# Kernel optimization log

Measured on AMD Instinct MI355X. Metric: run time of the kernel, lower is better.

Reference implementation:

```python
import jax, jax.numpy as jnp
import numpy as np

SEQ_LEN, BATCH, INPUT_SIZE, HIDDEN_SIZE = 512, 64, 1024, 1024


def setup_inputs() -> dict:
    key = jax.random.key(0)
    k1, k2, k3 = jax.random.split(key, 3)
    inp = jax.random.normal(k1, (SEQ_LEN, BATCH, INPUT_SIZE), dtype=jnp.float32)
    weight_ih = jax.random.normal(k2, (4 * HIDDEN_SIZE, INPUT_SIZE), dtype=jnp.float32) * 0.01
    weight_hh = jax.random.normal(k3, (4 * HIDDEN_SIZE, HIDDEN_SIZE), dtype=jnp.float32) * 0.01
    bias_ih = jnp.zeros((4 * HIDDEN_SIZE,), dtype=jnp.float32)
    bias_hh = jnp.zeros((4 * HIDDEN_SIZE,), dtype=jnp.float32)
    h0 = jnp.zeros((BATCH, HIDDEN_SIZE), dtype=jnp.float32)
    c0 = jnp.zeros((BATCH, HIDDEN_SIZE), dtype=jnp.float32)
    return {"input": inp, "weight_ih": weight_ih, "weight_hh": weight_hh,
            "bias_ih": bias_ih, "bias_hh": bias_hh, "h0": h0, "c0": c0}


def _lstm(input, weight_ih, weight_hh, bias_ih, bias_hh, h0, c0):
    H = weight_hh.shape[1]
    # Precompute input projections for all timesteps in one big GEMM: [T,B,4H]
    x_proj = jnp.einsum('tbi,gi->tbg', input, weight_ih) + bias_ih + bias_hh

    def step(carry, xg_t):
        h_prev, c_prev = carry
        gates = xg_t + h_prev @ weight_hh.T  # [B, 4H]
        i_g = jax.nn.sigmoid(gates[:, 0*H:1*H])
        f_g = jax.nn.sigmoid(gates[:, 1*H:2*H])
        g_g = jnp.tanh(gates[:, 2*H:3*H])
        o_g = jax.nn.sigmoid(gates[:, 3*H:4*H])
        c_cur = f_g * c_prev + i_g * g_g
        h_cur = o_g * jnp.tanh(c_cur)
        return (h_cur, c_cur), h_cur

    (h_last, c_last), outputs = jax.lax.scan(step, (h0, c0), x_proj)
    return outputs, (h_last[None], c_last[None])


def reference(input, weight_ih, weight_hh, bias_ih, bias_hh, h0, c0):
    return _lstm(input, weight_ih, weight_hh, bias_ih, bias_hh, h0, c0)
```

## Files before the change

kernel.cpp:

```cpp
#include <hip/hip_runtime.h>
#include <stdint.h>

#define SEQ    512
#define NBATCH 64
#define HID    1024
#define GDIM   4096

typedef __attribute__((ext_vector_type(4))) float          f32x4;
typedef __attribute__((ext_vector_type(8))) short          s16x8;
typedef __attribute__((ext_vector_type(4))) unsigned short u16x4;
typedef __attribute__((ext_vector_type(4))) unsigned int   u32x4;

#define MFMA_BF16(a,b,c) __builtin_amdgcn_mfma_f32_16x16x32_bf16((a),(b),(c),0,0,0)

__device__ __forceinline__ unsigned short f2bf(float f){
  union { float f; unsigned u; } v; v.f = f;
  unsigned r = v.u + 0x7fffu + ((v.u >> 16) & 1u);
  return (unsigned short)(r >> 16);
}

__device__ __forceinline__ void gload_lds16(const void* g, void* l){
  __builtin_amdgcn_global_load_lds((const __attribute__((address_space(1))) void*)g,
                                   (__attribute__((address_space(3))) void*)l,
                                   16, 0, 0);
}

__global__ __launch_bounds__(256) void cvt_bf16(const float* __restrict__ s,
                                                unsigned short* __restrict__ d, int n4){
  int i = blockIdx.x*256 + threadIdx.x;
  if (i >= n4) return;
  f32x4 v = *(const f32x4*)(s + (size_t)i*4);
  u16x4 o;
  o[0]=f2bf(v[0]); o[1]=f2bf(v[1]); o[2]=f2bf(v[2]); o[3]=f2bf(v[3]);
  *(u16x4*)(d + (size_t)i*4) = o;
}

__global__ __launch_bounds__(256) void init_state(const float* __restrict__ h0,
                                                  const float* __restrict__ c0,
                                                  unsigned short* __restrict__ hring,
                                                  float* __restrict__ cstate){
  int i = blockIdx.x*256 + threadIdx.x;
  hring[i]  = f2bf(h0[i]);
  cstate[i] = c0[i];
}

__global__ __launch_bounds__(256,1) void gemm_xproj(
    const unsigned short* __restrict__ A,
    const unsigned short* __restrict__ Bw,
    const float* __restrict__ bih, const float* __restrict__ bhh,
    float* __restrict__ C, int M)
{
  __shared__ unsigned short Al[2][128*64];
  __shared__ unsigned short Bl[2][128*64];

  const int bm = blockIdx.x >> 5;
  const int bn = blockIdx.x & 31;
  const int tid = threadIdx.x;
  const int wv = tid >> 6, l = tid & 63;
  const int wm = wv >> 1, wn = wv & 1;
  const int c16 = l & 15, rq = l >> 4;

  const unsigned short* Ab = A  + (size_t)bm*128*1024;
  const unsigned short* Bb = Bw + (size_t)bn*128*1024;

  f32x4 acc[4][4];
#pragma unroll
  for (int i=0;i<4;++i)
#pragma unroll
    for (int j=0;j<4;++j) acc[i][j] = (f32x4){0.f,0.f,0.f,0.f};

  auto stage = [&](int buf, int kt){
    const int k0 = kt*64;
    const int rsub = wv*8 + (l>>3);
    const int col  = (l&7)*8;
#pragma unroll
    for (int is=0; is<4; ++is){
      const int row = is*32 + rsub;
      gload_lds16(Ab + (size_t)row*1024 + k0 + col, &Al[buf][row*64 + col]);
      gload_lds16(Bb + (size_t)row*1024 + k0 + col, &Bl[buf][row*64 + col]);
    }
  };

  stage(0, 0);
  asm volatile("s_waitcnt vmcnt(0)" ::: "memory");
  __syncthreads();

  for (int kt = 0; kt < 16; ++kt){
    const int cur = kt & 1;
    if (kt < 15) stage(cur^1, kt+1);
#pragma unroll
    for (int ks=0; ks<2; ++ks){
      s16x8 afr[4], bfr[4];
#pragma unroll
      for (int mi=0;mi<4;++mi)
        afr[mi] = *(const s16x8*)&Al[cur][(wm*64 + mi*16 + c16)*64 + ks*32 + rq*8];
#pragma unroll
      for (int ni=0;ni<4;++ni)
        bfr[ni] = *(const s16x8*)&Bl[cur][(wn*64 + ni*16 + c16)*64 + ks*32 + rq*8];
#pragma unroll
      for (int mi=0;mi<4;++mi)
#pragma unroll
        for (int ni=0;ni<4;++ni)
          acc[mi][ni] = MFMA_BF16(afr[mi], bfr[ni], acc[mi][ni]);
    }
    asm volatile("s_waitcnt vmcnt(0)" ::: "memory");
    __syncthreads();
  }

  const int crow0 = bm*128 + wm*64;
  const int ccol0 = bn*128 + wn*64;
#pragma unroll
  for (int ni=0;ni<4;++ni){
    const int col = ccol0 + ni*16 + c16;
    const float bsum = bih[col] + bhh[col];
#pragma unroll
    for (int mi=0;mi<4;++mi){
      const int row = crow0 + mi*16 + rq*4;
#pragma unroll
      for (int r=0;r<4;++r)
        C[(size_t)(row+r)*GDIM + col] = acc[mi][ni][r] + bsum;
    }
  }
}

__global__ __launch_bounds__(512,1) void lstm_rec(
    const unsigned short* __restrict__ whhb,
    const float* __restrict__ xproj,
    unsigned short* __restrict__ hring,
    float* __restrict__ cstate,
    float* __restrict__ outp,
    unsigned int* __restrict__ bar,
    int t0, int nsteps)
{
  const int tid = threadIdx.x;
  const int wv = tid >> 6, l = tid & 63;
  const int kq = wv >> 1, rh = wv & 1;
  const int c16 = l & 15, rq = l >> 4;
  const int bq = blockIdx.x >> 6;
  const int hg = blockIdx.x & 63;
  const int hc0 = hg * 16;
  const int b0  = bq * 16;
  const int eb = tid >> 4, ec = tid & 15;
  const int sb = tid >> 5, cl0 = tid & 31;

  __shared__ s16x8 hls[16*128];
  __shared__ float part[8*16*36];
  __shared__ __align__(16) unsigned short hsh[16*16];

  s16x8 breg[2][8];
#pragma unroll
  for (int nt = 0; nt < 2; ++nt)
#pragma unroll
    for (int ks = 0; ks < 8; ++ks){
      const int n = rh*32 + nt*16 + c16;
      const int grow = (n & 3)*HID + hc0 + (n >> 2);
      const int k = kq*256 + ks*32 + rq*8;
      breg[nt][ks] = *(const s16x8*)(whhb + (size_t)grow*HID + k);
    }

  float creg = 0.f, xp[4] = {0.f,0.f,0.f,0.f};
  if (tid < 256){
    creg = cstate[(size_t)(b0+eb)*HID + hc0 + ec];
#pragma unroll
    for (int g = 0; g < 4; ++g)
      xp[g] = xproj[(size_t)(b0+eb)*GDIM + g*HID + hc0 + ec];
  }

  const unsigned int* myflag = bar + ((bq*64 + l) << 5);

  for (int t = t0; t < t0 + nsteps; ++t){
    if (wv == 0){
      unsigned fv; int spins = 0;
      const unsigned ut = (unsigned)t;
      do {
        asm volatile("global_load_dword %0, %1, off sc0 sc1\n\ts_waitcnt vmcnt(0)"
                     : "=v"(fv) : "v"(myflag) : "memory");
        if (fv >= ut) break;
        if (++spins > 4) __builtin_amdgcn_s_sleep(1);
      } while (spins < (1 << 17));
    }
    __syncthreads();

    {
      const unsigned short* gb = hring + (size_t)(t & 1)*65536
                               + (size_t)(b0 + sb)*HID;
      u32x4 tmp[4];
#pragma unroll
      for (int i = 0; i < 4; ++i){
        const unsigned short* p = gb + (cl0 + 32*i)*8;
        asm volatile("global_load_dwordx4 %0, %1, off sc0 sc1"
                     : "=v"(tmp[i]) : "v"(p));
      }
      asm volatile("s_waitcnt vmcnt(0)" ::: "memory");
      __builtin_amdgcn_sched_barrier(0);
#pragma unroll
      for (int i = 0; i < 4; ++i){
        const int cl = cl0 + 32*i;
        hls[sb*128 + ((cl & ~7) | ((cl & 7) ^ (sb & 7)))] =
            __builtin_bit_cast(s16x8, tmp[i]);
      }
    }
    __syncthreads();

    f32x4 acc0 = (f32x4){0.f,0.f,0.f,0.f};
    f32x4 acc1 = (f32x4){0.f,0.f,0.f,0.f};
    {
      s16x8 af[8];
#pragma unroll
      for (int ks = 0; ks < 8; ++ks){
        const int c = kq*32 + ks*4 + rq;
        af[ks] = hls[c16*128 + ((c & ~7) | ((c & 7) ^ (c16 & 7)))];
      }
#pragma unroll
      for (int ks = 0; ks < 8; ++ks){
        acc0 = MFMA_BF16(af[ks], breg[0][ks], acc0);
        acc1 = MFMA_BF16(af[ks], breg[1][ks], acc1);
      }
    }
#pragma unroll
    for (int r = 0; r < 4; ++r){
      part[wv*576 + (rq*4+r)*36 +      c16] = acc0[r];
      part[wv*576 + (rq*4+r)*36 + 16 + c16] = acc1[r];
    }
    __syncthreads();

    float hval = 0.f;
    if (tid < 256){
      float v[4];
#pragma unroll
      for (int g = 0; g < 4; ++g){
        const int row = ec*4 + g;
        const int pl = (row >> 5);
        const int nl = row & 31;
        v[g] = xp[g]
             + part[(0*2 + pl)*576 + eb*36 + nl]
             + part[(1*2 + pl)*576 + eb*36 + nl]
             + part[(2*2 + pl)*576 + eb*36 + nl]
             + part[(3*2 + pl)*576 + eb*36 + nl];
      }
      const float ig = 1.f/(1.f + __expf(-v[0]));
      const float fg = 1.f/(1.f + __expf(-v[1]));
      const float gg = tanhf(v[2]);
      const float og = 1.f/(1.f + __expf(-v[3]));
      creg = fg*creg + ig*gg;
      hval = og * tanhf(creg);
      hsh[eb*16 + ec] = f2bf(hval);
    }
    __syncthreads();

    if (tid < 32){
      const int row = tid >> 1, half = tid & 1;
      const unsigned short* hp = hring + (size_t)((t+1) & 1)*65536
                               + (size_t)(b0 + row)*HID + hc0 + half*8;
      u32x4 hv = *(const u32x4*)&hsh[row*16 + half*8];
      asm volatile("global_store_dwordx4 %0, %1, off sc0 sc1"
                   :: "v"(hp), "v"(hv) : "memory");
      asm volatile("s_waitcnt vmcnt(0)" ::: "memory");
      if (tid == 0){
        unsigned int* fp = bar + ((bq*64 + hg) << 5);
        unsigned int fv = (unsigned int)(t + 1);
        asm volatile("global_store_dword %0, %1, off sc0 sc1"
                     :: "v"(fp), "v"(fv) : "memory");
      }
    }

    if (tid < 256){
      const size_t oidx = (size_t)(b0+eb)*HID + hc0 + ec;
      outp[(size_t)t*65536 + oidx] = hval;
      if (t == SEQ-1){
        outp[(size_t)SEQ*65536 + oidx]         = hval;
        outp[(size_t)SEQ*65536 + 65536 + oidx] = creg;
      }
      if (t+1 < t0 + nsteps){
        const size_t xrow = (size_t)(t+1 - t0)*NBATCH + (b0+eb);
#pragma unroll
        for (int g = 0; g < 4; ++g)
          xp[g] = xproj[xrow*GDIM + g*HID + hc0 + ec];
      }
    }
  }

  if (tid < 256)
    cstate[(size_t)(b0+eb)*HID + hc0 + ec] = creg;
}

extern "C" void kernel_launch(void* const* d_in, const int* in_sizes, int n_in,
                              void* d_out, int out_size, void* d_ws, size_t ws_size,
                              hipStream_t stream)
{
  const float* inp = (const float*)d_in[0];
  const float* wih = (const float*)d_in[1];
  const float* whh = (const float*)d_in[2];
  const float* bih = (const float*)d_in[3];
  const float* bhh = (const float*)d_in[4];
  const float* h0  = (const float*)d_in[5];
  const float* c0  = (const float*)d_in[6];
  float* outp = (float*)d_out;

  auto alignup = [](size_t x){ return (x + 255) & ~(size_t)255; };
  auto need = [&](size_t ch)->size_t{
    size_t s = 0;
    s += alignup(ch*64*4096*4);
    s += alignup(ch*64*1024*2);
    s += alignup((size_t)4096*1024*2);
    s += alignup((size_t)4096*1024*2);
    s += alignup((size_t)2*64*1024*2);
    s += alignup((size_t)64*1024*4);
    s += alignup((size_t)256*32*4);
    return s;
  };
  int CH = 512;
  while (CH > 2 && need(CH) > ws_size) CH >>= 1;

  char* w = (char*)d_ws;
  float*          xproj  = (float*)w;          w += alignup((size_t)CH*64*4096*4);
  unsigned short* in_bf  = (unsigned short*)w; w += alignup((size_t)CH*64*1024*2);
  unsigned short* wih_bf = (unsigned short*)w; w += alignup((size_t)4096*1024*2);
  unsigned short* whh_bf = (unsigned short*)w; w += alignup((size_t)4096*1024*2);
  unsigned short* hring  = (unsigned short*)w; w += alignup((size_t)2*64*1024*2);
  float*          cst    = (float*)w;          w += alignup((size_t)64*1024*4);
  unsigned int*   bar    = (unsigned int*)w;

  hipMemsetAsync(bar, 0, 256*32*4, stream);

  cvt_bf16<<<4096, 256, 0, stream>>>(wih, wih_bf, 4096*1024/4);
  cvt_bf16<<<4096, 256, 0, stream>>>(whh, whh_bf, 4096*1024/4);
  init_state<<<256, 256, 0, stream>>>(h0, c0, hring, cst);

  const int nch = SEQ / CH;
  for (int ci = 0; ci < nch; ++ci){
    const int t0 = ci * CH;
    const int n4 = CH*64*1024/4;
    cvt_bf16<<<(n4+255)/256, 256, 0, stream>>>(inp + (size_t)t0*65536, in_bf, n4);
    gemm_xproj<<<dim3((CH*64/128)*32), 256, 0, stream>>>(in_bf, wih_bf, bih, bhh,
                                                         xproj, CH*64);
    lstm_rec<<<dim3(256), dim3(512), 0, stream>>>(whh_bf, xproj, hring, cst, outp,
                                                  bar, t0, CH);
  }
}
```

Baseline: 2.203 ms.

## Retile recurrent LSTM blocks to 8 batch rows by 32 hidden units

Each block of the persistent recurrent kernel now handles 8 batch rows and 32 hidden units instead of 16 and 16. Each wave now keeps twice as many W_hh fragments in registers and runs four MFMA tiles per k-step, with the unused half of the 16-row A tile zero-padded in LDS. Each block now polls only 32 producer flags and reads half as much of the h ring per step, which cuts the cross-block synchronisation and global h traffic per step. In exchange, register pressure doubles and half of every MFMA is spent on the padding rows.

```diff
diff --git a/kernel.cpp b/kernel.cpp
--- a/kernel.cpp
+++ b/kernel.cpp
@@ -136,40 +136,42 @@
   const int wv = tid >> 6, l = tid & 63;
   const int kq = wv >> 1, rh = wv & 1;
   const int c16 = l & 15, rq = l >> 4;
-  const int bq = blockIdx.x >> 6;
-  const int hg = blockIdx.x & 63;
-  const int hc0 = hg * 16;
-  const int b0  = bq * 16;
-  const int eb = tid >> 4, ec = tid & 15;
-  const int sb = tid >> 5, cl0 = tid & 31;
+  const int bq = blockIdx.x >> 5;
+  const int hg = blockIdx.x & 31;
+  const int hc0 = hg * 32;
+  const int b0  = bq * 8;
+  const int em = tid >> 5, ec = tid & 31;
+  const int sb = tid >> 6, scl = tid & 63;
 
   __shared__ s16x8 hls[16*128];
-  __shared__ float part[8*16*36];
-  __shared__ __align__(16) unsigned short hsh[16*16];
-
-  s16x8 breg[2][8];
-#pragma unroll
-  for (int nt = 0; nt < 2; ++nt)
-#pragma unroll
-    for (int ks = 0; ks < 8; ++ks){
-      const int n = rh*32 + nt*16 + c16;
-      const int grow = (n & 3)*HID + hc0 + (n >> 2);
-      const int k = kq*256 + ks*32 + rq*8;
-      breg[nt][ks] = *(const s16x8*)(whhb + (size_t)grow*HID + k);
-    }
+  __shared__ float part[4*8*4*33];
+  __shared__ __align__(16) unsigned short hsh[8*32];
+
+  s16x8 breg[4][8];
+#pragma unroll
+  for (int nt = 0; nt < 4; ++nt){
+    const int n = rh*64 + nt*16 + c16;
+    const size_t grow = (size_t)(n & 3)*HID + hc0 + (n >> 2);
+#pragma unroll
+    for (int ks = 0; ks < 8; ++ks)
+      breg[nt][ks] = *(const s16x8*)(whhb + grow*HID + kq*256 + ks*32 + rq*8);
+  }
+
+  hls[1024 + tid] = (s16x8){0,0,0,0,0,0,0,0};
+  hls[1536 + tid] = (s16x8){0,0,0,0,0,0,0,0};
 
   float creg = 0.f, xp[4] = {0.f,0.f,0.f,0.f};
   if (tid < 256){
-    creg = cstate[(size_t)(b0+eb)*HID + hc0 + ec];
+    creg = cstate[(size_t)(b0+em)*HID + hc0 + ec];
 #pragma unroll
     for (int g = 0; g < 4; ++g)
-      xp[g] = xproj[(size_t)(b0+eb)*GDIM + g*HID + hc0 + ec];
-  }
-
-  const unsigned int* myflag = bar + ((bq*64 + l) << 5);
+      xp[g] = xproj[(size_t)(b0+em)*GDIM + g*HID + hc0 + ec];
+  }
+
+  const unsigned int* myflag = bar + ((bq*32 + (l & 31)) << 5);
 
   for (int t = t0; t < t0 + nsteps; ++t){
-    if (wv == 0){
+    if (wv == 0 && l < 32){
       unsigned fv; int spins = 0;
       const unsigned ut = (unsigned)t;
       do {
@@ -184,43 +186,42 @@
     {
       const unsigned short* gb = hring + (size_t)(t & 1)*65536
                                + (size_t)(b0 + sb)*HID;
-      u32x4 tmp[4];
-#pragma unroll
-      for (int i = 0; i < 4; ++i){
-        const unsigned short* p = gb + (cl0 + 32*i)*8;
-        asm volatile("global_load_dwordx4 %0, %1, off sc0 sc1"
-                     : "=v"(tmp[i]) : "v"(p));
-      }
+      u32x4 t0v, t1v;
+      asm volatile("global_load_dwordx4 %0, %1, off sc0 sc1"
+                   : "=v"(t0v) : "v"(gb + scl*8));
+      asm volatile("global_load_dwordx4 %0, %1, off sc0 sc1"
+                   : "=v"(t1v) : "v"(gb + (scl + 64)*8));
       asm volatile("s_waitcnt vmcnt(0)" ::: "memory");
       __builtin_amdgcn_sched_barrier(0);
-#pragma unroll
-      for (int i = 0; i < 4; ++i){
-        const int cl = cl0 + 32*i;
-        hls[sb*128 + ((cl & ~7) | ((cl & 7) ^ (sb & 7)))] =
-            __builtin_bit_cast(s16x8, tmp[i]);
-      }
-    }
-    __syncthreads();
-
-    f32x4 acc0 = (f32x4){0.f,0.f,0.f,0.f};
-    f32x4 acc1 = (f32x4){0.f,0.f,0.f,0.f};
-    {
-      s16x8 af[8];
-#pragma unroll
-      for (int ks = 0; ks < 8; ++ks){
-        const int c = kq*32 + ks*4 + rq;
-        af[ks] = hls[c16*128 + ((c & ~7) | ((c & 7) ^ (c16 & 7)))];
-      }
-#pragma unroll
-      for (int ks = 0; ks < 8; ++ks){
-        acc0 = MFMA_BF16(af[ks], breg[0][ks], acc0);
-        acc1 = MFMA_BF16(af[ks], breg[1][ks], acc1);
-      }
-    }
-#pragma unroll
-    for (int r = 0; r < 4; ++r){
-      part[wv*576 + (rq*4+r)*36 +      c16] = acc0[r];
-      part[wv*576 + (rq*4+r)*36 + 16 + c16] = acc1[r];
+      const int c0 = scl, c1 = scl + 64;
+      hls[sb*128 + ((c0 & ~7) | ((c0 & 7) ^ (sb & 7)))] = __builtin_bit_cast(s16x8, t0v);
+      hls[sb*128 + ((c1 & ~7) | ((c1 & 7) ^ (sb & 7)))] = __builtin_bit_cast(s16x8, t1v);
+    }
+    __syncthreads();
+
+    f32x4 acc[4];
+#pragma unroll
+    for (int nt = 0; nt < 4; ++nt) acc[nt] = (f32x4){0.f,0.f,0.f,0.f};
+#pragma unroll
+    for (int ks = 0; ks < 8; ++ks){
+      const int c = kq*32 + ks*4 + rq;
+      const s16x8 af = hls[c16*128 + ((c & ~7) | ((c & 7) ^ (c16 & 7)))];
+#pragma unroll
+      for (int nt = 0; nt < 4; ++nt)
+        acc[nt] = MFMA_BF16(af, breg[nt][ks], acc[nt]);
+    }
+
+    if (rq < 2){
+#pragma unroll
+      for (int nt = 0; nt < 4; ++nt){
+        const int g = c16 & 3;
+        const int cl = rh*16 + nt*4 + (c16 >> 2);
+#pragma unroll
+        for (int r = 0; r < 4; ++r){
+          const int m = rq*4 + r;
+          part[((kq*8 + m)*4 + g)*33 + cl] = acc[nt][r];
+        }
+      }
     }
     __syncthreads();
 
@@ -229,14 +230,11 @@
       float v[4];
 #pragma unroll
       for (int g = 0; g < 4; ++g){
-        const int row = ec*4 + g;
-        const int pl = (row >> 5);
-        const int nl = row & 31;
         v[g] = xp[g]
-             + part[(0*2 + pl)*576 + eb*36 + nl]
-             + part[(1*2 + pl)*576 + eb*36 + nl]
-             + part[(2*2 + pl)*576 + eb*36 + nl]
-             + part[(3*2 + pl)*576 + eb*36 + nl];
+             + part[((0*8 + em)*4 + g)*33 + ec]
+             + part[((1*8 + em)*4 + g)*33 + ec]
+             + part[((2*8 + em)*4 + g)*33 + ec]
+             + part[((3*8 + em)*4 + g)*33 + ec];
       }
       const float ig = 1.f/(1.f + __expf(-v[0]));
       const float fg = 1.f/(1.f + __expf(-v[1]));
@@ -244,20 +242,20 @@
       const float og = 1.f/(1.f + __expf(-v[3]));
       creg = fg*creg + ig*gg;
       hval = og * tanhf(creg);
-      hsh[eb*16 + ec] = f2bf(hval);
+      hsh[em*32 + ec] = f2bf(hval);
     }
     __syncthreads();
 
     if (tid < 32){
-      const int row = tid >> 1, half = tid & 1;
+      const int row = tid >> 2, q = tid & 3;
       const unsigned short* hp = hring + (size_t)((t+1) & 1)*65536
-                               + (size_t)(b0 + row)*HID + hc0 + half*8;
-      u32x4 hv = *(const u32x4*)&hsh[row*16 + half*8];
+                               + (size_t)(b0 + row)*HID + hc0 + q*8;
+      u32x4 hv = *(const u32x4*)&hsh[row*32 + q*8];
       asm volatile("global_store_dwordx4 %0, %1, off sc0 sc1"
                    :: "v"(hp), "v"(hv) : "memory");
       asm volatile("s_waitcnt vmcnt(0)" ::: "memory");
       if (tid == 0){
-        unsigned int* fp = bar + ((bq*64 + hg) << 5);
+        unsigned int* fp = bar + ((bq*32 + hg) << 5);
         unsigned int fv = (unsigned int)(t + 1);
         asm volatile("global_store_dword %0, %1, off sc0 sc1"
                      :: "v"(fp), "v"(fv) : "memory");
@@ -265,14 +263,14 @@
     }
 
     if (tid < 256){
-      const size_t oidx = (size_t)(b0+eb)*HID + hc0 + ec;
+      const size_t oidx = (size_t)(b0+em)*HID + hc0 + ec;
       outp[(size_t)t*65536 + oidx] = hval;
       if (t == SEQ-1){
         outp[(size_t)SEQ*65536 + oidx]         = hval;
         outp[(size_t)SEQ*65536 + 65536 + oidx] = creg;
       }
       if (t+1 < t0 + nsteps){
-        const size_t xrow = (size_t)(t+1 - t0)*NBATCH + (b0+eb);
+        const size_t xrow = (size_t)(t+1 - t0)*NBATCH + (b0+em);
 #pragma unroll
         for (int g = 0; g < 4; ++g)
           xp[g] = xproj[xrow*GDIM + g*HID + hc0 + ec];
@@ -281,7 +279,7 @@
   }
 
   if (tid < 256)
-    cstate[(size_t)(b0+eb)*HID + hc0 + ec] = creg;
+    cstate[(size_t)(b0+em)*HID + hc0 + ec] = creg;
 }
 
 extern "C" void kernel_launch(void* const* d_in, const int* in_sizes, int n_in,
```

Measured after the change: 2.204 ms. No clear change (+0.0%).

## Fuse input projection into persistent LSTM recurrence kernel with register-resident W_ih

Applied to the files above, without the earlier changes.

Removes the separate xproj GEMM and its large fp32 intermediate buffer. Instead each recurrence block keeps its slice of W_ih in registers alongside W_hh and computes the next timestep's input projection with MFMA while the h ring is being published, double-buffering the partial sums in LDS. The goal is to eliminate the GEMM launch and the HBM round trip of xproj, and to hide the input-projection compute inside the recurrence's barrier wait. In exchange it doubles register pressure for weights, adds LDS use, and puts extra MFMA and global loads inside the serial per-step critical path.

```diff
diff --git a/kernel.cpp b/kernel.cpp
--- a/kernel.cpp
+++ b/kernel.cpp
@@ -17,12 +17,6 @@
   union { float f; unsigned u; } v; v.f = f;
   unsigned r = v.u + 0x7fffu + ((v.u >> 16) & 1u);
   return (unsigned short)(r >> 16);
-}
-
-__device__ __forceinline__ void gload_lds16(const void* g, void* l){
-  __builtin_amdgcn_global_load_lds((const __attribute__((address_space(1))) void*)g,
-                                   (__attribute__((address_space(3))) void*)l,
-                                   16, 0, 0);
 }
 
 __global__ __launch_bounds__(256) void cvt_bf16(const float* __restrict__ s,
@@ -44,88 +38,11 @@
   cstate[i] = c0[i];
 }
 
-__global__ __launch_bounds__(256,1) void gemm_xproj(
-    const unsigned short* __restrict__ A,
-    const unsigned short* __restrict__ Bw,
-    const float* __restrict__ bih, const float* __restrict__ bhh,
-    float* __restrict__ C, int M)
-{
-  __shared__ unsigned short Al[2][128*64];
-  __shared__ unsigned short Bl[2][128*64];
-
-  const int bm = blockIdx.x >> 5;
-  const int bn = blockIdx.x & 31;
-  const int tid = threadIdx.x;
-  const int wv = tid >> 6, l = tid & 63;
-  const int wm = wv >> 1, wn = wv & 1;
-  const int c16 = l & 15, rq = l >> 4;
-
-  const unsigned short* Ab = A  + (size_t)bm*128*1024;
-  const unsigned short* Bb = Bw + (size_t)bn*128*1024;
-
-  f32x4 acc[4][4];
-#pragma unroll
-  for (int i=0;i<4;++i)
-#pragma unroll
-    for (int j=0;j<4;++j) acc[i][j] = (f32x4){0.f,0.f,0.f,0.f};
-
-  auto stage = [&](int buf, int kt){
-    const int k0 = kt*64;
-    const int rsub = wv*8 + (l>>3);
-    const int col  = (l&7)*8;
-#pragma unroll
-    for (int is=0; is<4; ++is){
-      const int row = is*32 + rsub;
-      gload_lds16(Ab + (size_t)row*1024 + k0 + col, &Al[buf][row*64 + col]);
-      gload_lds16(Bb + (size_t)row*1024 + k0 + col, &Bl[buf][row*64 + col]);
-    }
-  };
-
-  stage(0, 0);
-  asm volatile("s_waitcnt vmcnt(0)" ::: "memory");
-  __syncthreads();
-
-  for (int kt = 0; kt < 16; ++kt){
-    const int cur = kt & 1;
-    if (kt < 15) stage(cur^1, kt+1);
-#pragma unroll
-    for (int ks=0; ks<2; ++ks){
-      s16x8 afr[4], bfr[4];
-#pragma unroll
-      for (int mi=0;mi<4;++mi)
-        afr[mi] = *(const s16x8*)&Al[cur][(wm*64 + mi*16 + c16)*64 + ks*32 + rq*8];
-#pragma unroll
-      for (int ni=0;ni<4;++ni)
-        bfr[ni] = *(const s16x8*)&Bl[cur][(wn*64 + ni*16 + c16)*64 + ks*32 + rq*8];
-#pragma unroll
-      for (int mi=0;mi<4;++mi)
-#pragma unroll
-        for (int ni=0;ni<4;++ni)
-          acc[mi][ni] = MFMA_BF16(afr[mi], bfr[ni], acc[mi][ni]);
-    }
-    asm volatile("s_waitcnt vmcnt(0)" ::: "memory");
-    __syncthreads();
-  }
-
-  const int crow0 = bm*128 + wm*64;
-  const int ccol0 = bn*128 + wn*64;
-#pragma unroll
-  for (int ni=0;ni<4;++ni){
-    const int col = ccol0 + ni*16 + c16;
-    const float bsum = bih[col] + bhh[col];
-#pragma unroll
-    for (int mi=0;mi<4;++mi){
-      const int row = crow0 + mi*16 + rq*4;
-#pragma unroll
-      for (int r=0;r<4;++r)
-        C[(size_t)(row+r)*GDIM + col] = acc[mi][ni][r] + bsum;
-    }
-  }
-}
-
 __global__ __launch_bounds__(512,1) void lstm_rec(
     const unsigned short* __restrict__ whhb,
-    const float* __restrict__ xproj,
+    const unsigned short* __restrict__ wihb,
+    const unsigned short* __restrict__ xbf,
+    const float* __restrict__ bih, const float* __restrict__ bhh,
     unsigned short* __restrict__ hring,
     float* __restrict__ cstate,
     float* __restrict__ outp,
@@ -145,28 +62,54 @@
 
   __shared__ s16x8 hls[16*128];
   __shared__ float part[8*16*36];
+  __shared__ float part_x[2*8*16*36];
   __shared__ __align__(16) unsigned short hsh[16*16];
 
-  s16x8 breg[2][8];
+  s16x8 breg[2][8], bihr[2][8];
 #pragma unroll
   for (int nt = 0; nt < 2; ++nt)
 #pragma unroll
     for (int ks = 0; ks < 8; ++ks){
       const int n = rh*32 + nt*16 + c16;
-      const int grow = (n & 3)*HID + hc0 + (n >> 2);
-      const int k = kq*256 + ks*32 + rq*8;
-      breg[nt][ks] = *(const s16x8*)(whhb + (size_t)grow*HID + k);
-    }
-
-  float creg = 0.f, xp[4] = {0.f,0.f,0.f,0.f};
+      const size_t off = ((size_t)(n & 3)*HID + hc0 + (n >> 2))*HID
+                       + kq*256 + ks*32 + rq*8;
+      breg[nt][ks] = *(const s16x8*)(whhb + off);
+      bihr[nt][ks] = *(const s16x8*)(wihb + off);
+    }
+
+  float creg = 0.f, bsum[4] = {0.f,0.f,0.f,0.f};
   if (tid < 256){
     creg = cstate[(size_t)(b0+eb)*HID + hc0 + ec];
 #pragma unroll
-    for (int g = 0; g < 4; ++g)
-      xp[g] = xproj[(size_t)(b0+eb)*GDIM + g*HID + hc0 + ec];
+    for (int g = 0; g < 4; ++g){
+      const size_t bi = (size_t)g*HID + hc0 + ec;
+      bsum[g] = bih[bi] + bhh[bi];
+    }
   }
 
   const unsigned int* myflag = bar + ((bq*64 + l) << 5);
+
+  {
+    const unsigned short* xb = xbf + ((size_t)t0*NBATCH + b0 + c16)*HID
+                             + kq*256 + rq*8;
+    s16x8 ax[8];
+#pragma unroll
+    for (int ks = 0; ks < 8; ++ks)
+      ax[ks] = *(const s16x8*)(xb + ks*32);
+    f32x4 ax0 = (f32x4){0.f,0.f,0.f,0.f};
+    f32x4 ax1 = (f32x4){0.f,0.f,0.f,0.f};
+#pragma unroll
+    for (int ks = 0; ks < 8; ++ks){
+      ax0 = MFMA_BF16(ax[ks], bihr[0][ks], ax0);
+      ax1 = MFMA_BF16(ax[ks], bihr[1][ks], ax1);
+    }
+    float* px = &part_x[(size_t)((t0 & 1)*8 + wv)*576];
+#pragma unroll
+    for (int r = 0; r < 4; ++r){
+      px[(rq*4+r)*36 +      c16] = ax0[r];
+      px[(rq*4+r)*36 + 16 + c16] = ax1[r];
+    }
+  }
 
   for (int t = t0; t < t0 + nsteps; ++t){
     if (wv == 0){
@@ -225,6 +168,7 @@
     __syncthreads();
 
     float hval = 0.f;
+    const int pxb = (t & 1)*8;
     if (tid < 256){
       float v[4];
 #pragma unroll
@@ -232,11 +176,15 @@
         const int row = ec*4 + g;
         const int pl = (row >> 5);
         const int nl = row & 31;
-        v[g] = xp[g]
+        v[g] = bsum[g]
              + part[(0*2 + pl)*576 + eb*36 + nl]
              + part[(1*2 + pl)*576 + eb*36 + nl]
              + part[(2*2 + pl)*576 + eb*36 + nl]
-             + part[(3*2 + pl)*576 + eb*36 + nl];
+             + part[(3*2 + pl)*576 + eb*36 + nl]
+             + part_x[(size_t)(pxb + 0*2 + pl)*576 + eb*36 + nl]
+             + part_x[(size_t)(pxb + 1*2 + pl)*576 + eb*36 + nl]
+             + part_x[(size_t)(pxb + 2*2 + pl)*576 + eb*36 + nl]
+             + part_x[(size_t)(pxb + 3*2 + pl)*576 + eb*36 + nl];
       }
       const float ig = 1.f/(1.f + __expf(-v[0]));
       const float fg = 1.f/(1.f + __expf(-v[1]));
@@ -248,19 +196,43 @@
     }
     __syncthreads();
 
-    if (tid < 32){
-      const int row = tid >> 1, half = tid & 1;
+    if (tid >= 448 && tid < 480){
+      const int i32 = tid - 448;
+      const int row = i32 >> 1, half = i32 & 1;
       const unsigned short* hp = hring + (size_t)((t+1) & 1)*65536
                                + (size_t)(b0 + row)*HID + hc0 + half*8;
       u32x4 hv = *(const u32x4*)&hsh[row*16 + half*8];
       asm volatile("global_store_dwordx4 %0, %1, off sc0 sc1"
                    :: "v"(hp), "v"(hv) : "memory");
       asm volatile("s_waitcnt vmcnt(0)" ::: "memory");
-      if (tid == 0){
+      if (i32 == 0){
         unsigned int* fp = bar + ((bq*64 + hg) << 5);
         unsigned int fv = (unsigned int)(t + 1);
         asm volatile("global_store_dword %0, %1, off sc0 sc1"
                      :: "v"(fp), "v"(fv) : "memory");
+      }
+    }
+
+    {
+      const int tn = (t+1 < SEQ) ? (t+1) : (SEQ-1);
+      const unsigned short* xb = xbf + ((size_t)tn*NBATCH + b0 + c16)*HID
+                               + kq*256 + rq*8;
+      s16x8 ax[8];
+#pragma unroll
+      for (int ks = 0; ks < 8; ++ks)
+        ax[ks] = *(const s16x8*)(xb + ks*32);
+      f32x4 ax0 = (f32x4){0.f,0.f,0.f,0.f};
+      f32x4 ax1 = (f32x4){0.f,0.f,0.f,0.f};
+#pragma unroll
+      for (int ks = 0; ks < 8; ++ks){
+        ax0 = MFMA_BF16(ax[ks], bihr[0][ks], ax0);
+        ax1 = MFMA_BF16(ax[ks], bihr[1][ks], ax1);
+      }
+      float* px = &part_x[(size_t)(((t+1) & 1)*8 + wv)*576];
+#pragma unroll
+      for (int r = 0; r < 4; ++r){
+        px[(rq*4+r)*36 +      c16] = ax0[r];
+        px[(rq*4+r)*36 + 16 + c16] = ax1[r];
       }
     }
 
@@ -270,12 +242,6 @@
       if (t == SEQ-1){
         outp[(size_t)SEQ*65536 + oidx]         = hval;
         outp[(size_t)SEQ*65536 + 65536 + oidx] = creg;
-      }
-      if (t+1 < t0 + nsteps){
-        const size_t xrow = (size_t)(t+1 - t0)*NBATCH + (b0+eb);
-#pragma unroll
-        for (int g = 0; g < 4; ++g)
-          xp[g] = xproj[xrow*GDIM + g*HID + hc0 + ec];
       }
     }
   }
@@ -298,23 +264,8 @@
   float* outp = (float*)d_out;
 
   auto alignup = [](size_t x){ return (x + 255) & ~(size_t)255; };
-  auto need = [&](size_t ch)->size_t{
-    size_t s = 0;
-    s += alignup(ch*64*4096*4);
-    s += alignup(ch*64*1024*2);
-    s += alignup((size_t)4096*1024*2);
-    s += alignup((size_t)4096*1024*2);
-    s += alignup((size_t)2*64*1024*2);
-    s += alignup((size_t)64*1024*4);
-    s += alignup((size_t)256*32*4);
-    return s;
-  };
-  int CH = 512;
-  while (CH > 2 && need(CH) > ws_size) CH >>= 1;
-
   char* w = (char*)d_ws;
-  float*          xproj  = (float*)w;          w += alignup((size_t)CH*64*4096*4);
-  unsigned short* in_bf  = (unsigned short*)w; w += alignup((size_t)CH*64*1024*2);
+  unsigned short* in_bf  = (unsigned short*)w; w += alignup((size_t)SEQ*64*1024*2);
   unsigned short* wih_bf = (unsigned short*)w; w += alignup((size_t)4096*1024*2);
   unsigned short* whh_bf = (unsigned short*)w; w += alignup((size_t)4096*1024*2);
   unsigned short* hring  = (unsigned short*)w; w += alignup((size_t)2*64*1024*2);
@@ -323,18 +274,11 @@
 
   hipMemsetAsync(bar, 0, 256*32*4, stream);
 
+  cvt_bf16<<<SEQ*64*1024/4/256, 256, 0, stream>>>(inp, in_bf, SEQ*64*1024/4);
   cvt_bf16<<<4096, 256, 0, stream>>>(wih, wih_bf, 4096*1024/4);
   cvt_bf16<<<4096, 256, 0, stream>>>(whh, whh_bf, 4096*1024/4);
   init_state<<<256, 256, 0, stream>>>(h0, c0, hring, cst);
 
-  const int nch = SEQ / CH;
-  for (int ci = 0; ci < nch; ++ci){
-    const int t0 = ci * CH;
-    const int n4 = CH*64*1024/4;
-    cvt_bf16<<<(n4+255)/256, 256, 0, stream>>>(inp + (size_t)t0*65536, in_bf, n4);
-    gemm_xproj<<<dim3((CH*64/128)*32), 256, 0, stream>>>(in_bf, wih_bf, bih, bhh,
-                                                         xproj, CH*64);
-    lstm_rec<<<dim3(256), dim3(512), 0, stream>>>(whh_bf, xproj, hring, cst, outp,
-                                                  bar, t0, CH);
-  }
-}
+  lstm_rec<<<dim3(256), dim3(512), 0, stream>>>(whh_bf, wih_bf, in_bf, bih, bhh,
+                                                hring, cst, outp, bar, 0, SEQ);
+}
```

Result: faster. 1.977 ms (-10.3%).
